# Kernel tuning notes

Hardware: AMD Instinct MI355X
Metric: run time of the kernel (lower is better)

Reference implementation:

```python
import jax, jax.numpy as jnp
import numpy as np

TOKENS, HIDDEN = 2048, 1024
N_EXPERTS, INTER, TOPK = 8, 2816, 2
RENORMALIZE = True


def setup_inputs() -> dict:
    key = jax.random.key(0)
    k1, k2, k3, k4 = jax.random.split(key, 4)
    x = jax.random.normal(k1, (TOKENS, HIDDEN), dtype=jnp.float32)
    gating_output = jax.random.normal(k2, (TOKENS, N_EXPERTS), dtype=jnp.float32)
    # stacked gate_proj+up_proj per expert: [E, 2*I, H]
    w1 = jax.random.normal(k3, (N_EXPERTS, 2 * INTER, HIDDEN), dtype=jnp.float32) * 0.02
    # down_proj per expert: [E, H, I]
    w2 = jax.random.normal(k4, (N_EXPERTS, HIDDEN, INTER), dtype=jnp.float32) * 0.02
    return {"x": x, "gating_output": gating_output, "w1": w1, "w2": w2}


def _moe(x, gating_output, w1, w2):
    # fused_topk: softmax over router logits, then top-k, then renormalize
    probs = jax.nn.softmax(gating_output, axis=-1)              # [T, E]
    topk_w, topk_ids = jax.lax.top_k(probs, TOPK)                # [T, K]
    if RENORMALIZE:
        topk_w = topk_w / jnp.sum(topk_w, axis=-1, keepdims=True)
    # fused_experts: gate/up proj -> SiLU(gate)*up -> down proj, per expert
    h = jnp.einsum('th,eih->tei', x, w1)                         # [T, E, 2I]
    gate, up = h[..., :INTER], h[..., INTER:]
    act = jax.nn.silu(gate) * up                                 # [T, E, I]
    out_e = jnp.einsum('tei,ehi->teh', act, w2)                  # [T, E, H]
    # combine: gather selected experts and weight them
    sel = jnp.take_along_axis(out_e, topk_ids[:, :, None], axis=1)  # [T, K, H]
    return jnp.sum(sel * topk_w[:, :, None].astype(sel.dtype), axis=1)  # [T, H]


def reference(x, gating_output, w1, w2):
    return _moe(x, gating_output, w1, w2)
```

## Files before the change

kernel.cpp:

```cpp
#include <hip/hip_runtime.h>
#include <hip/hip_bf16.h>

#define TOKENS 2048
#define HIDDEN 1024
#define NEXP   8
#define INTER  2816
#define N1     5632
#define ROWCAP 5120
#define SPLITK 2

typedef __attribute__((ext_vector_type(8))) short short8;
typedef __attribute__((ext_vector_type(4))) float f32x4;

typedef unsigned int __attribute__((address_space(1))) as1_uint;
typedef unsigned int __attribute__((address_space(3))) as3_uint;

__device__ __forceinline__ void gload16(const void* g, void* l) {
  __builtin_amdgcn_global_load_lds((const as1_uint*)g, (as3_uint*)l, 16, 0, 0);
}

__device__ __forceinline__ unsigned short f2bf(float f) {
  unsigned u = __float_as_uint(f);
  u += 0x7fff + ((u >> 16) & 1);
  return (unsigned short)(u >> 16);
}
__device__ __forceinline__ float bf2f(unsigned short h) {
  return __uint_as_float(((unsigned)h) << 16);
}
__device__ __forceinline__ unsigned short bfs(float x) {
  __hip_bfloat16 h = __float2bfloat16(x);
  return *reinterpret_cast<unsigned short*>(&h);
}
__device__ __forceinline__ short8 pack8(f32x4 lo, f32x4 hi) {
  short8 o;
  o[0] = (short)bfs(lo[0]); o[1] = (short)bfs(lo[1]); o[2] = (short)bfs(lo[2]); o[3] = (short)bfs(lo[3]);
  o[4] = (short)bfs(hi[0]); o[5] = (short)bfs(hi[1]); o[6] = (short)bfs(hi[2]); o[7] = (short)bfs(hi[3]);
  return o;
}

__global__ void k_routing(const float* __restrict__ gate, int* __restrict__ ctrl,
                          int* __restrict__ tkid, float* __restrict__ tkw) {
  int t = blockIdx.x * blockDim.x + threadIdx.x;
  if (t >= TOKENS) return;
  float l[8];
#pragma unroll
  for (int i = 0; i < 8; i++) l[i] = gate[t * 8 + i];
  int i0 = 0; float m0 = l[0];
#pragma unroll
  for (int i = 1; i < 8; i++) if (l[i] > m0) { m0 = l[i]; i0 = i; }
  int i1 = -1; float m1 = -3.4e38f;
#pragma unroll
  for (int i = 0; i < 8; i++) if (i != i0 && l[i] > m1) { m1 = l[i]; i1 = i; }
  float e  = __expf(m1 - m0);
  float w0 = 1.f / (1.f + e);
  float w1 = e / (1.f + e);
  tkid[2 * t] = i0; tkid[2 * t + 1] = i1;
  tkw[2 * t] = w0;  tkw[2 * t + 1] = w1;
  atomicAdd(&ctrl[i0], 1);
  atomicAdd(&ctrl[i1], 1);
}

__global__ void k_base(int* ctrl) {
  if (threadIdx.x == 0) {
    int a = 0;
    for (int e = 0; e < 8; e++) { ctrl[16 + e] = a; a += ((ctrl[e] + 127) >> 7) << 7; }
  }
}

__global__ void k_fill(int* __restrict__ ctrl, const int* __restrict__ tkid,
                       int* __restrict__ rtok, int* __restrict__ trow) {
  int t = blockIdx.x * blockDim.x + threadIdx.x;
  if (t >= TOKENS) return;
#pragma unroll
  for (int k = 0; k < 2; k++) {
    int e = tkid[2 * t + k];
    int pos = atomicAdd(&ctrl[8 + e], 1);
    int row = ctrl[16 + e] + pos;
    rtok[row] = t;
    trow[2 * t + k] = row;
  }
}

__global__ void k_gather(const float* __restrict__ x, const int* __restrict__ ctrl,
                         const int* __restrict__ rtok, unsigned short* __restrict__ Abf) {
  int row = blockIdx.x;
  int e = -1, local = 0;
  for (int i = 0; i < 8; i++) {
    int b = ctrl[16 + i], p = ((ctrl[i] + 127) >> 7) << 7;
    if (row >= b && row < b + p) { e = i; local = row - b; break; }
  }
  if (e < 0) return;
  int tid = threadIdx.x;
  unsigned short* dst = Abf + (size_t)row * HIDDEN;
  if (local < ctrl[e]) {
    int t = rtok[row];
    float4 v = ((const float4*)(x + (size_t)t * HIDDEN))[tid];
    ushort4 o; o.x = f2bf(v.x); o.y = f2bf(v.y); o.z = f2bf(v.z); o.w = f2bf(v.w);
    ((ushort4*)dst)[tid] = o;
  } else {
    ushort4 z; z.x = 0; z.y = 0; z.z = 0; z.w = 0;
    ((ushort4*)dst)[tid] = z;
  }
}

__device__ __forceinline__ int tile_lookup(const int* ctrl, int mt, int* ml) {
  int a0 = 0;
  for (int i = 0; i < 8; i++) {
    int pt = (ctrl[i] + 127) >> 7;
    if (mt < a0 + pt) { *ml = mt - a0; return i; }
    a0 += pt;
  }
  return -1;
}

__global__ __launch_bounds__(256, 3) void k_gemm1(const float* __restrict__ w1,
    const unsigned short* __restrict__ Abf, unsigned short* __restrict__ act,
    const int* __restrict__ ctrl) {
  union __align__(16) LdsU {
    struct { unsigned char A[16384]; unsigned char B[32768]; } st;
    unsigned short hb[128 * 132];
  };
  __shared__ LdsU lds;
  int mt = blockIdx.y, ml;
  int e = tile_lookup(ctrl, mt, &ml);
  if (e < 0) return;
  int nt = blockIdx.x;
  int tid = threadIdx.x, lane = tid & 63, wid = tid >> 6, wr = wid >> 1, wc = wid & 1;
  int rbase = ctrl[16 + e] + ml * 128;
  const unsigned char* Ab = (const unsigned char*)(Abf + (size_t)rbase * HIDDEN);
  const unsigned char* Bb = (const unsigned char*)(w1 + (size_t)e * N1 * HIDDEN);
  int swzA = ((lane & 7) ^ (lane >> 3)) << 4;
  int l3 = lane >> 3;
  int l4 = lane >> 4;

  f32x4 acc[4][4];
  f32x4 zero = {0.f, 0.f, 0.f, 0.f};
#pragma unroll
  for (int i = 0; i < 4; i++)
#pragma unroll
    for (int j = 0; j < 4; j++) acc[i][j] = zero;

  for (int kk = 0; kk < HIDDEN / 64; ++kk) {
#pragma unroll
    for (int i = 0; i < 4; i++) {
      int g = wid * 4 + i;
      gload16(Ab + (size_t)(g * 8 + l3) * (HIDDEN * 2) + kk * 128 + swzA, &lds.st.A[g * 1024]);
    }
#pragma unroll
    for (int i = 0; i < 8; i++) {
      int g = wid * 8 + i;
      int r = g * 4 + l4;
      int grow = (r < 64) ? (nt * 64 + r) : (INTER + nt * 64 + r - 64);
      int jsrc = ((lane & 15) ^ (r & 7)) << 4;
      gload16(Bb + (size_t)grow * (HIDDEN * 4) + kk * 256 + jsrc, &lds.st.B[g * 1024]);
    }
    __syncthreads();
#pragma unroll
    for (int ks = 0; ks < 2; ++ks) {
      short8 a[4], b[4];
#pragma unroll
      for (int mi = 0; mi < 4; mi++) {
        int row = wr * 64 + mi * 16 + (lane & 15);
        int koff = ks * 64 + (l4 << 4);
        a[mi] = *(const short8*)&lds.st.A[row * 128 + (koff ^ ((row & 7) << 4))];
      }
#pragma unroll
      for (int ni = 0; ni < 4; ni++) {
        int r = wc * 64 + ni * 16 + (lane & 15);
        int b0 = ks * 8 + (l4 << 1);
        f32x4 lo = *(const f32x4*)&lds.st.B[r * 256 + ((b0 ^ (r & 7)) << 4)];
        f32x4 hi = *(const f32x4*)&lds.st.B[r * 256 + (((b0 + 1) ^ (r & 7)) << 4)];
        b[ni] = pack8(lo, hi);
      }
#pragma unroll
      for (int mi = 0; mi < 4; mi++)
#pragma unroll
        for (int ni = 0; ni < 4; ni++)
          acc[mi][ni] = __builtin_amdgcn_mfma_f32_16x16x32_bf16(a[mi], b[ni], acc[mi][ni], 0, 0, 0);
    }
    __syncthreads();
  }
#pragma unroll
  for (int mi = 0; mi < 4; mi++)
#pragma unroll
    for (int ni = 0; ni < 4; ni++)
#pragma unroll
      for (int r = 0; r < 4; r++) {
        int row = wr * 64 + mi * 16 + ((lane >> 4) << 2) + r;
        int col = wc * 64 + ni * 16 + (lane & 15);
        lds.hb[row * 132 + col] = f2bf(acc[mi][ni][r]);
      }
  __syncthreads();
  {
    int r = tid >> 1, ch = (tid & 1) * 32;
    unsigned short* orow = act + (size_t)(rbase + r) * INTER + nt * 64 + ch;
    const unsigned short* hrow = &lds.hb[r * 132];
#pragma unroll
    for (int j = 0; j < 32; j += 4) {
      ushort4 o;
#pragma unroll
      for (int q = 0; q < 4; q++) {
        float g = bf2f(hrow[ch + j + q]);
        float u = bf2f(hrow[64 + ch + j + q]);
        float s = g / (1.f + __expf(-g));
        ((unsigned short*)&o)[q] = f2bf(s * u);
      }
      *(ushort4*)(orow + j) = o;
    }
  }
}

__global__ __launch_bounds__(256, 3) void k_gemm2(const float* __restrict__ w2,
    const unsigned short* __restrict__ act, float* __restrict__ P0, float* __restrict__ P1,
    const int* __restrict__ ctrl) {
  struct __align__(16) Lds2 { unsigned char A[16384]; unsigned char B[32768]; };
  __shared__ Lds2 lds;
  int mt = blockIdx.y, ml;
  int e = tile_lookup(ctrl, mt, &ml);
  if (e < 0) return;
  int nt = blockIdx.x;
  int z  = blockIdx.z;
  int tid = threadIdx.x, lane = tid & 63, wid = tid >> 6, wr = wid >> 1, wc = wid & 1;
  int rbase = ctrl[16 + e] + ml * 128;
  const unsigned char* Ab = (const unsigned char*)(act + (size_t)rbase * INTER);
  const unsigned char* Bb = (const unsigned char*)(w2 + (size_t)e * HIDDEN * INTER);
  int swzA = ((lane & 7) ^ (lane >> 3)) << 4;
  int l3 = lane >> 3, l4 = lane >> 4;
  const int KST = (INTER / 64) / SPLITK;

  f32x4 acc[4][4];
  f32x4 zero = {0.f, 0.f, 0.f, 0.f};
#pragma unroll
  for (int i = 0; i < 4; i++)
#pragma unroll
    for (int j = 0; j < 4; j++) acc[i][j] = zero;

  for (int s = 0; s < KST; ++s) {
    int kk = z * KST + s;
#pragma unroll
    for (int i = 0; i < 4; i++) {
      int g = wid * 4 + i;
      gload16(Ab + (size_t)(g * 8 + l3) * (INTER * 2) + kk * 128 + swzA, &lds.A[g * 1024]);
    }
#pragma unroll
    for (int i = 0; i < 8; i++) {
      int g = wid * 8 + i;
      int r = g * 4 + l4;
      int jsrc = ((lane & 15) ^ (r & 7)) << 4;
      gload16(Bb + (size_t)(nt * 128 + r) * (INTER * 4) + kk * 256 + jsrc, &lds.B[g * 1024]);
    }
    __syncthreads();
#pragma unroll
    for (int ks = 0; ks < 2; ++ks) {
      short8 a[4], b[4];
#pragma unroll
      for (int mi = 0; mi < 4; mi++) {
        int row = wr * 64 + mi * 16 + (lane & 15);
        int koff = ks * 64 + (l4 << 4);
        a[mi] = *(const short8*)&lds.A[row * 128 + (koff ^ ((row & 7) << 4))];
      }
#pragma unroll
      for (int ni = 0; ni < 4; ni++) {
        int r = wc * 64 + ni * 16 + (lane & 15);
        int b0 = ks * 8 + (l4 << 1);
        f32x4 lo = *(const f32x4*)&lds.B[r * 256 + ((b0 ^ (r & 7)) << 4)];
        f32x4 hi = *(const f32x4*)&lds.B[r * 256 + (((b0 + 1) ^ (r & 7)) << 4)];
        b[ni] = pack8(lo, hi);
      }
#pragma unroll
      for (int mi = 0; mi < 4; mi++)
#pragma unroll
        for (int ni = 0; ni < 4; ni++)
          acc[mi][ni] = __builtin_amdgcn_mfma_f32_16x16x32_bf16(a[mi], b[ni], acc[mi][ni], 0, 0, 0);
    }
    __syncthreads();
  }
  float* P = z ? P1 : P0;
#pragma unroll
  for (int mi = 0; mi < 4; mi++)
#pragma unroll
    for (int ni = 0; ni < 4; ni++) {
      int col = nt * 128 + wc * 64 + ni * 16 + (lane & 15);
#pragma unroll
      for (int r = 0; r < 4; r++) {
        int row = rbase + wr * 64 + mi * 16 + ((lane >> 4) << 2) + r;
        P[(size_t)row * HIDDEN + col] = acc[mi][ni][r];
      }
    }
}

__global__ void k_finish(const float* __restrict__ P0, const float* __restrict__ P1,
                         const int* __restrict__ trow, const float* __restrict__ tkw,
                         float* __restrict__ out) {
  int t = blockIdx.x, c = threadIdx.x;
  int r0 = trow[2 * t], r1 = trow[2 * t + 1];
  float w0 = tkw[2 * t], w1 = tkw[2 * t + 1];
  float4 a0 = ((const float4*)(P0 + (size_t)r0 * HIDDEN))[c];
  float4 b0 = ((const float4*)(P1 + (size_t)r0 * HIDDEN))[c];
  float4 a1 = ((const float4*)(P0 + (size_t)r1 * HIDDEN))[c];
  float4 b1 = ((const float4*)(P1 + (size_t)r1 * HIDDEN))[c];
  float4 o;
  o.x = w0 * (a0.x + b0.x) + w1 * (a1.x + b1.x);
  o.y = w0 * (a0.y + b0.y) + w1 * (a1.y + b1.y);
  o.z = w0 * (a0.z + b0.z) + w1 * (a1.z + b1.z);
  o.w = w0 * (a0.w + b0.w) + w1 * (a1.w + b1.w);
  ((float4*)(out + (size_t)t * HIDDEN))[c] = o;
}

extern "C" void kernel_launch(void* const* d_in, const int* in_sizes, int n_in,
                              void* d_out, int out_size, void* d_ws, size_t ws_size,
                              hipStream_t stream) {
  const float* x      = (const float*)d_in[0];
  const float* gating = (const float*)d_in[1];
  const float* w1     = (const float*)d_in[2];
  const float* w2     = (const float*)d_in[3];
  float* out = (float*)d_out;
  char* ws = (char*)d_ws;

  int*   ctrl = (int*)ws;
  int*   tkid = (int*)(ws + 1024);
  float* tkw  = (float*)(ws + 17408);
  int*   rtok = (int*)(ws + 33792);
  int*   trow = (int*)(ws + 54272);
  size_t off_Abf = 131072;
  size_t off_act = off_Abf + (size_t)ROWCAP * HIDDEN * 2;
  size_t off_P0  = off_act + (size_t)ROWCAP * INTER * 2;
  size_t off_P1  = off_P0  + (size_t)ROWCAP * HIDDEN * 4;
  unsigned short* Abf  = (unsigned short*)(ws + off_Abf);
  unsigned short* actb = (unsigned short*)(ws + off_act);
  float* P0 = (float*)(ws + off_P0);
  float* P1 = (float*)(ws + off_P1);

  hipMemsetAsync(ws, 0, 1024, stream);

  k_routing<<<TOKENS / 256, 256, 0, stream>>>(gating, ctrl, tkid, tkw);
  k_base<<<1, 64, 0, stream>>>(ctrl);
  k_fill<<<TOKENS / 256, 256, 0, stream>>>(ctrl, tkid, rtok, trow);
  k_gather<<<ROWCAP, 256, 0, stream>>>(x, ctrl, rtok, Abf);
  k_gemm1<<<dim3(N1 / 128, 40), 256, 0, stream>>>(w1, Abf, actb, ctrl);
  k_gemm2<<<dim3(HIDDEN / 128, 40, SPLITK), 256, 0, stream>>>(w2, actb, P0, P1, ctrl);
  k_finish<<<TOKENS, 256, 0, stream>>>(P0, P1, trow, tkw, out);
}
```

Baseline: 243.3 us.

## Enlarge MoE GEMM tiles to 256 rows and convert weights to bf16 once in LDS

Both expert GEMMs move from 128-row, 256-thread tiles to 256-row, 512-thread tiles, with per-expert padding raised to 256 rows. Each fp32 weight tile is converted to bf16 once into a swizzled LDS buffer, instead of every wave re-packing it inside the MFMA loop. The next weight slice is prefetched while the current one is computed. Grids are flattened with an XCD-interleaved block mapping. The aim is to halve weight re-reads from HBM and remove redundant conversion work. The cost is more padding rows, higher LDS use per block and an extra barrier per k-step.

```diff
diff --git a/kernel.cpp b/kernel.cpp
--- a/kernel.cpp
+++ b/kernel.cpp
@@ -6,7 +6,10 @@
 #define NEXP   8
 #define INTER  2816
 #define N1     5632
-#define ROWCAP 5120
+#define ROWCAP 6144
+#define MT     24
+#define NT1    44
+#define NT2    8
 #define SPLITK 2
 
 typedef __attribute__((ext_vector_type(8))) short short8;
@@ -30,12 +33,6 @@
 __device__ __forceinline__ unsigned short bfs(float x) {
   __hip_bfloat16 h = __float2bfloat16(x);
   return *reinterpret_cast<unsigned short*>(&h);
-}
-__device__ __forceinline__ short8 pack8(f32x4 lo, f32x4 hi) {
-  short8 o;
-  o[0] = (short)bfs(lo[0]); o[1] = (short)bfs(lo[1]); o[2] = (short)bfs(lo[2]); o[3] = (short)bfs(lo[3]);
-  o[4] = (short)bfs(hi[0]); o[5] = (short)bfs(hi[1]); o[6] = (short)bfs(hi[2]); o[7] = (short)bfs(hi[3]);
-  return o;
 }
 
 __global__ void k_routing(const float* __restrict__ gate, int* __restrict__ ctrl,
@@ -63,7 +60,7 @@
 __global__ void k_base(int* ctrl) {
   if (threadIdx.x == 0) {
     int a = 0;
-    for (int e = 0; e < 8; e++) { ctrl[16 + e] = a; a += ((ctrl[e] + 127) >> 7) << 7; }
+    for (int e = 0; e < 8; e++) { ctrl[16 + e] = a; a += ((ctrl[e] + 255) >> 8) << 8; }
   }
 }
 
@@ -86,7 +83,7 @@
   int row = blockIdx.x;
   int e = -1, local = 0;
   for (int i = 0; i < 8; i++) {
-    int b = ctrl[16 + i], p = ((ctrl[i] + 127) >> 7) << 7;
+    int b = ctrl[16 + i], p = ((ctrl[i] + 255) >> 8) << 8;
     if (row >= b && row < b + p) { e = i; local = row - b; break; }
   }
   if (e < 0) return;
@@ -106,32 +103,42 @@
 __device__ __forceinline__ int tile_lookup(const int* ctrl, int mt, int* ml) {
   int a0 = 0;
   for (int i = 0; i < 8; i++) {
-    int pt = (ctrl[i] + 127) >> 7;
+    int pt = (ctrl[i] + 255) >> 8;
     if (mt < a0 + pt) { *ml = mt - a0; return i; }
     a0 += pt;
   }
   return -1;
 }
 
-__global__ __launch_bounds__(256, 3) void k_gemm1(const float* __restrict__ w1,
+__global__ __launch_bounds__(512, 4) void k_gemm1(const float* __restrict__ w1,
     const unsigned short* __restrict__ Abf, unsigned short* __restrict__ act,
     const int* __restrict__ ctrl) {
   union __align__(16) LdsU {
-    struct { unsigned char A[16384]; unsigned char B[32768]; } st;
-    unsigned short hb[128 * 132];
+    struct { unsigned char A[32768]; unsigned char Bf[32768]; unsigned char Bb[16384]; } st;
+    unsigned short hb[256 * 132];
   };
   __shared__ LdsU lds;
-  int mt = blockIdx.y, ml;
-  int e = tile_lookup(ctrl, mt, &ml);
+  int bid = blockIdx.x;
+  int wg = (bid & 7) * (NT1 * MT / 8) + (bid >> 3);
+  int mt = wg / NT1, nt = wg % NT1;
+  int ml; int e = tile_lookup(ctrl, mt, &ml);
   if (e < 0) return;
-  int nt = blockIdx.x;
   int tid = threadIdx.x, lane = tid & 63, wid = tid >> 6, wr = wid >> 1, wc = wid & 1;
-  int rbase = ctrl[16 + e] + ml * 128;
+  int rbase = ctrl[16 + e] + ml * 256;
   const unsigned char* Ab = (const unsigned char*)(Abf + (size_t)rbase * HIDDEN);
-  const unsigned char* Bb = (const unsigned char*)(w1 + (size_t)e * N1 * HIDDEN);
-  int swzA = ((lane & 7) ^ (lane >> 3)) << 4;
-  int l3 = lane >> 3;
-  int l4 = lane >> 4;
+  const unsigned char* Bw = (const unsigned char*)(w1 + (size_t)e * N1 * HIDDEN);
+  int l3 = lane >> 3, l4 = lane >> 4, l15 = lane & 15;
+  int swzA = ((lane & 7) ^ l3) << 4;
+
+  size_t aoff[4], boff[4];
+#pragma unroll
+  for (int i = 0; i < 4; i++) {
+    int g = wid * 4 + i;
+    aoff[i] = (size_t)(g * 8 + l3) * (HIDDEN * 2) + swzA;
+    int r = g * 4 + l4;
+    int grow = (r < 64) ? nt * 64 + r : INTER + nt * 64 + (r - 64);
+    boff[i] = (size_t)grow * (HIDDEN * 4) + (size_t)l15 * 16;
+  }
 
   f32x4 acc[4][4];
   f32x4 zero = {0.f, 0.f, 0.f, 0.f};
@@ -140,37 +147,46 @@
 #pragma unroll
     for (int j = 0; j < 4; j++) acc[i][j] = zero;
 
-  for (int kk = 0; kk < HIDDEN / 64; ++kk) {
+#pragma unroll
+  for (int i = 0; i < 4; i++)
+    gload16(Bw + boff[i], &lds.st.Bf[(wid * 4 + i) * 1024]);
+
+  const int NS = HIDDEN / 64;
+  for (int s = 0; s < NS; ++s) {
+#pragma unroll
+    for (int i = 0; i < 4; i++)
+      gload16(Ab + aoff[i] + s * 128, &lds.st.A[(wid * 4 + i) * 1024]);
+    __syncthreads();
 #pragma unroll
     for (int i = 0; i < 4; i++) {
-      int g = wid * 4 + i;
-      gload16(Ab + (size_t)(g * 8 + l3) * (HIDDEN * 2) + kk * 128 + swzA, &lds.st.A[g * 1024]);
-    }
-#pragma unroll
-    for (int i = 0; i < 8; i++) {
-      int g = wid * 8 + i;
-      int r = g * 4 + l4;
-      int grow = (r < 64) ? (nt * 64 + r) : (INTER + nt * 64 + r - 64);
-      int jsrc = ((lane & 15) ^ (r & 7)) << 4;
-      gload16(Bb + (size_t)grow * (HIDDEN * 4) + kk * 256 + jsrc, &lds.st.B[g * 1024]);
-    }
-    __syncthreads();
+      int off = wid * 4096 + i * 1024 + lane * 16;
+      f32x4 v = *(const f32x4*)&lds.st.Bf[off];
+      int r = off >> 8, jL = (off >> 4) & 15;
+      uint2 wv;
+      wv.x = (unsigned)bfs(v[0]) | ((unsigned)bfs(v[1]) << 16);
+      wv.y = (unsigned)bfs(v[2]) | ((unsigned)bfs(v[3]) << 16);
+      *(uint2*)&lds.st.Bb[r * 128 + ((((jL >> 1) ^ (r & 7)) << 4) | ((jL & 1) << 3))] = wv;
+    }
+    __syncthreads();
+    if (s + 1 < NS) {
+#pragma unroll
+      for (int i = 0; i < 4; i++)
+        gload16(Bw + boff[i] + (size_t)(s + 1) * 256, &lds.st.Bf[(wid * 4 + i) * 1024]);
+    }
 #pragma unroll
     for (int ks = 0; ks < 2; ++ks) {
       short8 a[4], b[4];
 #pragma unroll
       for (int mi = 0; mi < 4; mi++) {
-        int row = wr * 64 + mi * 16 + (lane & 15);
+        int row = wr * 64 + mi * 16 + l15;
         int koff = ks * 64 + (l4 << 4);
         a[mi] = *(const short8*)&lds.st.A[row * 128 + (koff ^ ((row & 7) << 4))];
       }
 #pragma unroll
       for (int ni = 0; ni < 4; ni++) {
-        int r = wc * 64 + ni * 16 + (lane & 15);
-        int b0 = ks * 8 + (l4 << 1);
-        f32x4 lo = *(const f32x4*)&lds.st.B[r * 256 + ((b0 ^ (r & 7)) << 4)];
-        f32x4 hi = *(const f32x4*)&lds.st.B[r * 256 + (((b0 + 1) ^ (r & 7)) << 4)];
-        b[ni] = pack8(lo, hi);
+        int row = wc * 64 + ni * 16 + l15;
+        int koff = ks * 64 + (l4 << 4);
+        b[ni] = *(const short8*)&lds.st.Bb[row * 128 + (koff ^ ((row & 7) << 4))];
       }
 #pragma unroll
       for (int mi = 0; mi < 4; mi++)
@@ -186,8 +202,8 @@
     for (int ni = 0; ni < 4; ni++)
 #pragma unroll
       for (int r = 0; r < 4; r++) {
-        int row = wr * 64 + mi * 16 + ((lane >> 4) << 2) + r;
-        int col = wc * 64 + ni * 16 + (lane & 15);
+        int row = wr * 64 + mi * 16 + (l4 << 2) + r;
+        int col = wc * 64 + ni * 16 + l15;
         lds.hb[row * 132 + col] = f2bf(acc[mi][ni][r]);
       }
   __syncthreads();
@@ -210,23 +226,34 @@
   }
 }
 
-__global__ __launch_bounds__(256, 3) void k_gemm2(const float* __restrict__ w2,
-    const unsigned short* __restrict__ act, float* __restrict__ P0, float* __restrict__ P1,
+__global__ __launch_bounds__(512, 4) void k_gemm2(const float* __restrict__ w2,
+    const unsigned short* __restrict__ act, float* __restrict__ Pb,
     const int* __restrict__ ctrl) {
-  struct __align__(16) Lds2 { unsigned char A[16384]; unsigned char B[32768]; };
+  struct __align__(16) Lds2 { unsigned char A[32768]; unsigned char Bf[32768]; unsigned char Bb[16384]; };
   __shared__ Lds2 lds;
-  int mt = blockIdx.y, ml;
-  int e = tile_lookup(ctrl, mt, &ml);
+  int bid = blockIdx.x;
+  int wg = (bid & 7) * (NT2 * MT * SPLITK / 8) + (bid >> 3);
+  int z = wg / (MT * NT2);
+  int rem = wg % (MT * NT2);
+  int mt = rem >> 3, nt = rem & 7;
+  int ml; int e = tile_lookup(ctrl, mt, &ml);
   if (e < 0) return;
-  int nt = blockIdx.x;
-  int z  = blockIdx.z;
   int tid = threadIdx.x, lane = tid & 63, wid = tid >> 6, wr = wid >> 1, wc = wid & 1;
-  int rbase = ctrl[16 + e] + ml * 128;
-  const unsigned char* Ab = (const unsigned char*)(act + (size_t)rbase * INTER);
-  const unsigned char* Bb = (const unsigned char*)(w2 + (size_t)e * HIDDEN * INTER);
-  int swzA = ((lane & 7) ^ (lane >> 3)) << 4;
-  int l3 = lane >> 3, l4 = lane >> 4;
+  int rbase = ctrl[16 + e] + ml * 256;
   const int KST = (INTER / 64) / SPLITK;
+  const unsigned char* Ab = (const unsigned char*)(act + (size_t)rbase * INTER) + (size_t)z * KST * 128;
+  const unsigned char* Bw = (const unsigned char*)(w2 + (size_t)e * HIDDEN * INTER) + (size_t)z * KST * 256;
+  int l3 = lane >> 3, l4 = lane >> 4, l15 = lane & 15;
+  int swzA = ((lane & 7) ^ l3) << 4;
+
+  size_t aoff[4], boff[4];
+#pragma unroll
+  for (int i = 0; i < 4; i++) {
+    int g = wid * 4 + i;
+    aoff[i] = (size_t)(g * 8 + l3) * (INTER * 2) + swzA;
+    int r = g * 4 + l4;
+    boff[i] = (size_t)(nt * 128 + r) * (INTER * 4) + (size_t)l15 * 16;
+  }
 
   f32x4 acc[4][4];
   f32x4 zero = {0.f, 0.f, 0.f, 0.f};
@@ -235,37 +262,45 @@
 #pragma unroll
     for (int j = 0; j < 4; j++) acc[i][j] = zero;
 
+#pragma unroll
+  for (int i = 0; i < 4; i++)
+    gload16(Bw + boff[i], &lds.Bf[(wid * 4 + i) * 1024]);
+
   for (int s = 0; s < KST; ++s) {
-    int kk = z * KST + s;
+#pragma unroll
+    for (int i = 0; i < 4; i++)
+      gload16(Ab + aoff[i] + s * 128, &lds.A[(wid * 4 + i) * 1024]);
+    __syncthreads();
 #pragma unroll
     for (int i = 0; i < 4; i++) {
-      int g = wid * 4 + i;
-      gload16(Ab + (size_t)(g * 8 + l3) * (INTER * 2) + kk * 128 + swzA, &lds.A[g * 1024]);
-    }
-#pragma unroll
-    for (int i = 0; i < 8; i++) {
-      int g = wid * 8 + i;
-      int r = g * 4 + l4;
-      int jsrc = ((lane & 15) ^ (r & 7)) << 4;
-      gload16(Bb + (size_t)(nt * 128 + r) * (INTER * 4) + kk * 256 + jsrc, &lds.B[g * 1024]);
-    }
-    __syncthreads();
+      int off = wid * 4096 + i * 1024 + lane * 16;
+      f32x4 v = *(const f32x4*)&lds.Bf[off];
+      int r = off >> 8, jL = (off >> 4) & 15;
+      uint2 wv;
+      wv.x = (unsigned)bfs(v[0]) | ((unsigned)bfs(v[1]) << 16);
+      wv.y = (unsigned)bfs(v[2]) | ((unsigned)bfs(v[3]) << 16);
+      *(uint2*)&lds.Bb[r * 128 + ((((jL >> 1) ^ (r & 7)) << 4) | ((jL & 1) << 3))] = wv;
+    }
+    __syncthreads();
+    if (s + 1 < KST) {
+#pragma unroll
+      for (int i = 0; i < 4; i++)
+        gload16(Bw + boff[i] + (size_t)(s + 1) * 256, &lds.Bf[(wid * 4 + i) * 1024]);
+    }
 #pragma unroll
     for (int ks = 0; ks < 2; ++ks) {
       short8 a[4], b[4];
 #pragma unroll
       for (int mi = 0; mi < 4; mi++) {
-        int row = wr * 64 + mi * 16 + (lane & 15);
+        int row = wr * 64 + mi * 16 + l15;
         int koff = ks * 64 + (l4 << 4);
         a[mi] = *(const short8*)&lds.A[row * 128 + (koff ^ ((row & 7) << 4))];
       }
 #pragma unroll
       for (int ni = 0; ni < 4; ni++) {
-        int r = wc * 64 + ni * 16 + (lane & 15);
-        int b0 = ks * 8 + (l4 << 1);
-        f32x4 lo = *(const f32x4*)&lds.B[r * 256 + ((b0 ^ (r & 7)) << 4)];
-        f32x4 hi = *(const f32x4*)&lds.B[r * 256 + (((b0 + 1) ^ (r & 7)) << 4)];
-        b[ni] = pack8(lo, hi);
+        int row = wc * 64 + ni * 16 + l15;
+        int koff = ks * 64 + (l4 << 4);
+        b[ni] = *(const short8*)&lds.Bb[row * 128 + (koff ^ ((row & 7) << 4))];
       }
 #pragma unroll
       for (int mi = 0; mi < 4; mi++)
@@ -275,24 +310,26 @@
     }
     __syncthreads();
   }
-  float* P = z ? P1 : P0;
+  float* P = Pb + (size_t)z * ROWCAP * HIDDEN;
 #pragma unroll
   for (int mi = 0; mi < 4; mi++)
 #pragma unroll
     for (int ni = 0; ni < 4; ni++) {
-      int col = nt * 128 + wc * 64 + ni * 16 + (lane & 15);
+      int col = nt * 128 + wc * 64 + ni * 16 + l15;
 #pragma unroll
       for (int r = 0; r < 4; r++) {
-        int row = rbase + wr * 64 + mi * 16 + ((lane >> 4) << 2) + r;
+        int row = rbase + wr * 64 + mi * 16 + (l4 << 2) + r;
         P[(size_t)row * HIDDEN + col] = acc[mi][ni][r];
       }
     }
 }
 
-__global__ void k_finish(const float* __restrict__ P0, const float* __restrict__ P1,
+__global__ void k_finish(const float* __restrict__ Pb,
                          const int* __restrict__ trow, const float* __restrict__ tkw,
                          float* __restrict__ out) {
   int t = blockIdx.x, c = threadIdx.x;
+  const float* P0 = Pb;
+  const float* P1 = Pb + (size_t)ROWCAP * HIDDEN;
   int r0 = trow[2 * t], r1 = trow[2 * t + 1];
   float w0 = tkw[2 * t], w1 = tkw[2 * t + 1];
   float4 a0 = ((const float4*)(P0 + (size_t)r0 * HIDDEN))[c];
@@ -318,18 +355,16 @@
   char* ws = (char*)d_ws;
 
   int*   ctrl = (int*)ws;
-  int*   tkid = (int*)(ws + 1024);
-  float* tkw  = (float*)(ws + 17408);
-  int*   rtok = (int*)(ws + 33792);
-  int*   trow = (int*)(ws + 54272);
+  int*   tkid = (int*)(ws + 4096);
+  float* tkw  = (float*)(ws + 24576);
+  int*   rtok = (int*)(ws + 45056);
+  int*   trow = (int*)(ws + 73728);
   size_t off_Abf = 131072;
   size_t off_act = off_Abf + (size_t)ROWCAP * HIDDEN * 2;
-  size_t off_P0  = off_act + (size_t)ROWCAP * INTER * 2;
-  size_t off_P1  = off_P0  + (size_t)ROWCAP * HIDDEN * 4;
+  size_t off_P   = off_act + (size_t)ROWCAP * INTER * 2;
   unsigned short* Abf  = (unsigned short*)(ws + off_Abf);
   unsigned short* actb = (unsigned short*)(ws + off_act);
-  float* P0 = (float*)(ws + off_P0);
-  float* P1 = (float*)(ws + off_P1);
+  float* Pb = (float*)(ws + off_P);
 
   hipMemsetAsync(ws, 0, 1024, stream);
 
@@ -337,7 +372,7 @@
   k_base<<<1, 64, 0, stream>>>(ctrl);
   k_fill<<<TOKENS / 256, 256, 0, stream>>>(ctrl, tkid, rtok, trow);
   k_gather<<<ROWCAP, 256, 0, stream>>>(x, ctrl, rtok, Abf);
-  k_gemm1<<<dim3(N1 / 128, 40), 256, 0, stream>>>(w1, Abf, actb, ctrl);
-  k_gemm2<<<dim3(HIDDEN / 128, 40, SPLITK), 256, 0, stream>>>(w2, actb, P0, P1, ctrl);
-  k_finish<<<TOKENS, 256, 0, stream>>>(P0, P1, trow, tkw, out);
-}
+  k_gemm1<<<NT1 * MT, 512, 0, stream>>>(w1, Abf, actb, ctrl);
+  k_gemm2<<<NT2 * MT * SPLITK, 512, 0, stream>>>(w2, actb, Pb, ctrl);
+  k_finish<<<TOKENS, 256, 0, stream>>>(Pb, trow, tkw, out);
+}
```

Result: no change. 243.6 us (+0.2%).
